# Kernel tuning notes

Hardware: AMD Instinct MI355X
Metric: run time of the kernel (lower is better)

## Reference

```python
import jax, jax.numpy as jnp
import numpy as np

N_LEAVES = 8192      # perfect binary tree, depth 13
SEQ_SIZE = 4096
EMBED = 512
NUM_CLASSES = 2


def setup_inputs() -> dict:
    key = jax.random.key(0)
    ks = jax.random.split(key, 7)
    sc = lambda n: 1.0 / np.sqrt(n)
    return {
        "leaf_seq": jax.random.normal(ks[0], (N_LEAVES, SEQ_SIZE), jnp.float32),
        # nn.Linear(sequenceSize, embedSize)
        "W_emb": jax.random.normal(ks[1], (EMBED, SEQ_SIZE), jnp.float32) * sc(SEQ_SIZE),
        "b_emb": jax.random.normal(ks[2], (EMBED,), jnp.float32) * 0.01,
        # nn.Linear(2*embedSize, embedSize)
        "W_comb": jax.random.normal(ks[3], (EMBED, 2 * EMBED), jnp.float32) * sc(2 * EMBED),
        "b_comb": jax.random.normal(ks[4], (EMBED,), jnp.float32) * 0.01,
        # nn.Linear(embedSize, numClasses)
        "W_proj": jax.random.normal(ks[5], (NUM_CLASSES, EMBED), jnp.float32) * sc(EMBED),
        "b_proj": jax.random.normal(ks[6], (NUM_CLASSES,), jnp.float32) * 0.01,
    }


def reference(leaf_seq, W_emb, b_emb, W_comb, b_comb, W_proj, b_proj):
    # Depth-batched version of the recursive traverse():
    # leaves: h = relu(embedding(seq))  -- one big GEMM instead of N batch-1 calls
    h = jax.nn.relu(leaf_seq @ W_emb.T + b_emb)            # [N_LEAVES, E]
    # internal nodes: h = relu(W(cat(left, right))), one GEMM per tree level.
    # Leaves 2i and 2i+1 are siblings (in-order perfect binary tree layout),
    # matching cat((traverse(child0), traverse(child1)), dim=1).
    while h.shape[0] > 1:                                   # fixed 13 levels at trace time
        pair = jnp.concatenate([h[0::2], h[1::2]], axis=1)  # [n/2, 2E]
        h = jax.nn.relu(pair @ W_comb.T + b_comb)           # [n/2, E]
    # root only: projection(currentNode) -> nodeProbList, cat -> [1, numClasses]
    return h @ W_proj.T + b_proj
```

## Files before the change

kernel.cpp:

```cpp
#include <hip/hip_runtime.h>
#include <stdint.h>


typedef float  f32x16 __attribute__((ext_vector_type(16)));
typedef short  s16x8  __attribute__((ext_vector_type(8)));
typedef unsigned short u16;

__device__ __forceinline__ u16 f2bf_rne(float f) {
    union { float f; uint32_t u; } v; v.f = f;
    return (u16)((v.u + 0x7FFFu + ((v.u >> 16) & 1u)) >> 16);
}
__device__ __forceinline__ float bf2f(u16 h) {
    union { uint32_t u; float f; } v; v.u = ((uint32_t)h) << 16;
    return v.f;
}
__device__ __forceinline__ void split2(float f, u16& h, u16& l) {
    union { float f; uint32_t u; } v; v.f = f;
    h = (u16)(v.u >> 16);
    union { uint32_t u; float f; } hf; hf.u = v.u & 0xFFFF0000u;
    l = f2bf_rne(f - hf.f);
}

__device__ __forceinline__ int swz(int row, int p, int e) {
    return (row * 128 + p * 64 + e) ^ ((row & 15) << 3);
}

__global__ __launch_bounds__(256) void split_kernel(
    const float* __restrict__ x, u16* __restrict__ hi, u16* __restrict__ lo, int n4)
{
    int i = blockIdx.x * 256 + threadIdx.x;
    if (i >= n4) return;
    float4 v = ((const float4*)x)[i];
    ushort4 h, l;
    split2(v.x, h.x, l.x);
    split2(v.y, h.y, l.y);
    split2(v.z, h.z, l.z);
    split2(v.w, h.w, l.w);
    ((ushort4*)hi)[i] = h;
    ((ushort4*)lo)[i] = l;
}

__global__ __launch_bounds__(256, 1) void gemm_emb(
    const float* __restrict__ Af,
    const u16* __restrict__ Bhi_g, const u16* __restrict__ Blo_g,
    const float* __restrict__ bias,
    u16* __restrict__ Chi, u16* __restrict__ Clo)
{
    constexpr int K = 4096, N = 512;
    __shared__ u16 Asw[128 * 128];
    __shared__ u16 Bsw[128 * 128];

    const int tid = threadIdx.x, wid = tid >> 6, lane = tid & 63;
    const int mb = blockIdx.x * 128, nb = blockIdx.y * 128;
    const int wm = (wid >> 1) * 64, wn = (wid & 1) * 64;
    const int sr = tid >> 1;
    const int se = (tid & 1) * 32;

    const float* pA  = Af    + (long)(mb + sr) * K + se;
    const u16*   pBh = Bhi_g + (long)(nb + sr) * K + se;
    const u16*   pBl = Blo_g + (long)(nb + sr) * K + se;

    f32x16 accA[2][2] = {};
    f32x16 accB[2][2] = {};
    float4 ra[8];
    s16x8  rbh[4], rbl[4];

    auto fetch = [&](int k0) {
#pragma unroll
        for (int i = 0; i < 8; ++i) ra[i] = *(const float4*)(pA + k0 + 4 * i);
#pragma unroll
        for (int i = 0; i < 4; ++i) {
            rbh[i] = *(const s16x8*)(pBh + k0 + 8 * i);
            rbl[i] = *(const s16x8*)(pBl + k0 + 8 * i);
        }
    };
    auto stage = [&]() {
#pragma unroll
        for (int q = 0; q < 4; ++q) {
            s16x8 hh, ll;
#pragma unroll
            for (int j = 0; j < 8; ++j) {
                float f = (j < 4) ? (&ra[2 * q].x)[j] : (&ra[2 * q + 1].x)[j - 4];
                u16 h, l; split2(f, h, l);
                hh[j] = (short)h; ll[j] = (short)l;
            }
            *(s16x8*)&Asw[swz(sr, 0, se + 8 * q)] = hh;
            *(s16x8*)&Asw[swz(sr, 1, se + 8 * q)] = ll;
            *(s16x8*)&Bsw[swz(sr, 0, se + 8 * q)] = rbh[q];
            *(s16x8*)&Bsw[swz(sr, 1, se + 8 * q)] = rbl[q];
        }
    };

    fetch(0);
    const int fr = lane & 31, ko = lane >> 5;
    for (int k0 = 0; k0 < K; k0 += 64) {
        stage();
        __syncthreads();
        if (k0 + 64 < K) fetch(k0 + 64);
#pragma unroll
        for (int s = 0; s < 4; ++s) {
            const int e = s * 16 + ko * 8;
            s16x8 ah[2], al[2], bh[2], bl[2];
#pragma unroll
            for (int i = 0; i < 2; ++i) {
                ah[i] = *(const s16x8*)&Asw[swz(wm + 32 * i + fr, 0, e)];
                al[i] = *(const s16x8*)&Asw[swz(wm + 32 * i + fr, 1, e)];
                bh[i] = *(const s16x8*)&Bsw[swz(wn + 32 * i + fr, 0, e)];
                bl[i] = *(const s16x8*)&Bsw[swz(wn + 32 * i + fr, 1, e)];
            }
#pragma unroll
            for (int i = 0; i < 2; ++i)
#pragma unroll
                for (int j = 0; j < 2; ++j) {
                    accA[i][j] = __builtin_amdgcn_mfma_f32_32x32x16_bf16(ah[i], bh[j], accA[i][j], 0, 0, 0);
                    accA[i][j] = __builtin_amdgcn_mfma_f32_32x32x16_bf16(al[i], bh[j], accA[i][j], 0, 0, 0);
                    accB[i][j] = __builtin_amdgcn_mfma_f32_32x32x16_bf16(ah[i], bl[j], accB[i][j], 0, 0, 0);
                }
        }
        __syncthreads();
    }

    const int fc = lane & 31;
#pragma unroll
    for (int i = 0; i < 2; ++i)
#pragma unroll
        for (int j = 0; j < 2; ++j) {
            const int col = nb + wn + 32 * j + fc;
            const float bv = bias[col];
#pragma unroll
            for (int reg = 0; reg < 16; ++reg) {
                const int row = mb + wm + 32 * i + (reg & 3) + 8 * (reg >> 2) + 4 * (lane >> 5);
                float v = fmaxf(accA[i][j][reg] + accB[i][j][reg] + bv, 0.f);
                u16 h = f2bf_rne(v);
                const long idx = (long)row * N + col;
                Chi[idx] = h;
                Clo[idx] = f2bf_rne(v - bf2f(h));
            }
        }
}

__global__ __launch_bounds__(256, 2) void gemm_cmb(
    const u16* __restrict__ Ahi, const u16* __restrict__ Alo,
    const u16* __restrict__ Whi, const u16* __restrict__ Wlo,
    const float* __restrict__ bias,
    u16* __restrict__ Ohi, u16* __restrict__ Olo,
    int m)
{
    constexpr int K = 1024, N = 512;
    __shared__ u16 Asw[64 * 128];
    __shared__ u16 Bsw[128 * 128];

    const int tid = threadIdx.x, wid = tid >> 6, lane = tid & 63;
    const int mb = blockIdx.x * 64, nb = blockIdx.y * 128;
    const int wm = (wid >> 1) * 32, wn = (wid & 1) * 64;
    const int ar = tid >> 2, ae = (tid & 3) * 16;
    const int br = tid >> 1, be = (tid & 1) * 32;
    const bool aval = (mb + ar) < m;
    const long aoff = (long)(mb + ar) * K + ae;
    const long boff = (long)(nb + br) * K + be;

    f32x16 accA[2] = {};
    f32x16 accB[2] = {};
    const s16x8 zz = {0, 0, 0, 0, 0, 0, 0, 0};
    s16x8 rah[2], ral[2], rbh[4], rbl[4];

    auto fetch = [&](int k0) {
        if (aval) {
            rah[0] = *(const s16x8*)(Ahi + aoff + k0);
            rah[1] = *(const s16x8*)(Ahi + aoff + k0 + 8);
            ral[0] = *(const s16x8*)(Alo + aoff + k0);
            ral[1] = *(const s16x8*)(Alo + aoff + k0 + 8);
        } else {
            rah[0] = zz; rah[1] = zz; ral[0] = zz; ral[1] = zz;
        }
#pragma unroll
        for (int i = 0; i < 4; ++i) {
            rbh[i] = *(const s16x8*)(Whi + boff + k0 + 8 * i);
            rbl[i] = *(const s16x8*)(Wlo + boff + k0 + 8 * i);
        }
    };
    auto stage = [&]() {
#pragma unroll
        for (int q = 0; q < 2; ++q) {
            *(s16x8*)&Asw[swz(ar, 0, ae + 8 * q)] = rah[q];
            *(s16x8*)&Asw[swz(ar, 1, ae + 8 * q)] = ral[q];
        }
#pragma unroll
        for (int q = 0; q < 4; ++q) {
            *(s16x8*)&Bsw[swz(br, 0, be + 8 * q)] = rbh[q];
            *(s16x8*)&Bsw[swz(br, 1, be + 8 * q)] = rbl[q];
        }
    };

    fetch(0);
    const int fr = lane & 31, ko = lane >> 5;
    for (int k0 = 0; k0 < K; k0 += 64) {
        stage();
        __syncthreads();
        if (k0 + 64 < K) fetch(k0 + 64);
#pragma unroll
        for (int s = 0; s < 4; ++s) {
            const int e = s * 16 + ko * 8;
            s16x8 ah = *(const s16x8*)&Asw[swz(wm + fr, 0, e)];
            s16x8 al = *(const s16x8*)&Asw[swz(wm + fr, 1, e)];
#pragma unroll
            for (int j = 0; j < 2; ++j) {
                s16x8 bh = *(const s16x8*)&Bsw[swz(wn + 32 * j + fr, 0, e)];
                s16x8 bl = *(const s16x8*)&Bsw[swz(wn + 32 * j + fr, 1, e)];
                accA[j] = __builtin_amdgcn_mfma_f32_32x32x16_bf16(ah, bh, accA[j], 0, 0, 0);
                accA[j] = __builtin_amdgcn_mfma_f32_32x32x16_bf16(al, bh, accA[j], 0, 0, 0);
                accB[j] = __builtin_amdgcn_mfma_f32_32x32x16_bf16(ah, bl, accB[j], 0, 0, 0);
            }
        }
        __syncthreads();
    }

    const int fc = lane & 31;
#pragma unroll
    for (int j = 0; j < 2; ++j) {
        const int col = nb + wn + 32 * j + fc;
        const float bv = bias[col];
#pragma unroll
        for (int reg = 0; reg < 16; ++reg) {
            const int row = mb + wm + (reg & 3) + 8 * (reg >> 2) + 4 * (lane >> 5);
            if (row < m) {
                float v = fmaxf(accA[j][reg] + accB[j][reg] + bv, 0.f);
                u16 h = f2bf_rne(v);
                const long idx = (long)row * N + col;
                Ohi[idx] = h;
                Olo[idx] = f2bf_rne(v - bf2f(h));
            }
        }
    }
}

__global__ __launch_bounds__(256) void tail_gemv(
    const u16* __restrict__ Hhi, const u16* __restrict__ Hlo,
    const float* __restrict__ W,
    const float* __restrict__ bias,
    u16* __restrict__ Ohi, u16* __restrict__ Olo)
{
    __shared__ float hrow[1024];
    const int row = blockIdx.x;
    const int tid = threadIdx.x;
    const int n   = blockIdx.y * 256 + tid;

    ushort4 hv = ((const ushort4*)(Hhi + (long)row * 1024))[tid];
    ushort4 lv = ((const ushort4*)(Hlo + (long)row * 1024))[tid];
    hrow[4 * tid + 0] = bf2f(hv.x) + bf2f(lv.x);
    hrow[4 * tid + 1] = bf2f(hv.y) + bf2f(lv.y);
    hrow[4 * tid + 2] = bf2f(hv.z) + bf2f(lv.z);
    hrow[4 * tid + 3] = bf2f(hv.w) + bf2f(lv.w);
    __syncthreads();

    const float* w = W + (long)n * 1024;
    float s = 0.f;
#pragma unroll 8
    for (int k = 0; k < 1024; k += 4) {
        float4 wv = *(const float4*)(w + k);
        s = fmaf(hrow[k + 0], wv.x, s);
        s = fmaf(hrow[k + 1], wv.y, s);
        s = fmaf(hrow[k + 2], wv.z, s);
        s = fmaf(hrow[k + 3], wv.w, s);
    }
    float v = fmaxf(s + bias[n], 0.f);
    u16 h = f2bf_rne(v);
    Ohi[(long)row * 512 + n] = h;
    Olo[(long)row * 512 + n] = f2bf_rne(v - bf2f(h));
}

__global__ __launch_bounds__(128) void proj_kernel(
    const u16* __restrict__ hhi, const u16* __restrict__ hlo,
    const float* __restrict__ W, const float* __restrict__ b, float* __restrict__ out)
{
    const int c    = threadIdx.x >> 6;
    const int lane = threadIdx.x & 63;
    float s = 0.f;
#pragma unroll
    for (int j = 0; j < 8; ++j) {
        const int idx = lane + 64 * j;
        s = fmaf(bf2f(hhi[idx]) + bf2f(hlo[idx]), W[c * 512 + idx], s);
    }
#pragma unroll
    for (int off = 32; off > 0; off >>= 1) s += __shfl_down(s, off);
    if (lane == 0) out[c] = s + b[c];
}

extern "C" void kernel_launch(void* const* d_in, const int* in_sizes, int n_in,
                              void* d_out, int out_size, void* d_ws, size_t ws_size,
                              hipStream_t stream)
{
    const float* leaf   = (const float*)d_in[0];
    const float* W_emb  = (const float*)d_in[1];
    const float* b_emb  = (const float*)d_in[2];
    const float* W_comb = (const float*)d_in[3];
    const float* b_comb = (const float*)d_in[4];
    const float* W_proj = (const float*)d_in[5];
    const float* b_proj = (const float*)d_in[6];
    float* out = (float*)d_out;

    u16* p = (u16*)d_ws;
    u16* WembHi  = p; p += (size_t)512 * 4096;
    u16* WembLo  = p; p += (size_t)512 * 4096;
    u16* WcombHi = p; p += (size_t)512 * 1024;
    u16* WcombLo = p; p += (size_t)512 * 1024;
    u16* h0h = p; p += (size_t)8192 * 512;
    u16* h0l = p; p += (size_t)8192 * 512;
    u16* h1h = p; p += (size_t)4096 * 512;
    u16* h1l = p; p += (size_t)4096 * 512;

    {
        int n4 = 512 * 4096 / 4;
        split_kernel<<<(n4 + 255) / 256, 256, 0, stream>>>(W_emb, WembHi, WembLo, n4);
        n4 = 512 * 1024 / 4;
        split_kernel<<<(n4 + 255) / 256, 256, 0, stream>>>(W_comb, WcombHi, WcombLo, n4);
    }

    gemm_emb<<<dim3(64, 4), 256, 0, stream>>>(
        leaf, WembHi, WembLo, b_emb, h0h, h0l);

    u16 *ih = h0h, *il = h0l, *oh = h1h, *ol = h1l;
    for (int m = 4096; m >= 64; m >>= 1) {
        gemm_cmb<<<dim3((m + 63) / 64, 4), 256, 0, stream>>>(
            ih, il, WcombHi, WcombLo, b_comb, oh, ol, m);
        u16* t;
        t = ih; ih = oh; oh = t;
        t = il; il = ol; ol = t;
    }

    for (int m = 32; m >= 1; m >>= 1) {
        tail_gemv<<<dim3(m, 2), 256, 0, stream>>>(
            ih, il, W_comb, b_comb, oh, ol);
        u16* t;
        t = ih; ih = oh; oh = t;
        t = il; il = ol; ol = t;
    }

    proj_kernel<<<1, 128, 0, stream>>>(ih, il, W_proj, b_proj, out);
}
```

Baseline: 727.4 us.

## Split-K embedding GEMM with atomics and rewrite combine GEMM as register split-K

The embedding GEMM is split into two K halves across a third grid dimension. Partial sums go into a zeroed fp32 buffer through atomic adds, and a separate reduce kernel applies bias, ReLU and the hi/lo split. The combine GEMM is rewritten to load operands straight from global memory into registers, with each wave owning a quarter of K and an LDS reduction at the end. It also uses 64x64 output tiles, so all levels down to m=1 go through the MFMA path and the tail GEMV kernels are removed. This aims to raise parallelism on the 256-block embedding GEMM and the small late levels, at the cost of atomic traffic, a memset, an extra reduce pass, workspace aliasing, and combine-kernel loads that no longer go through LDS.

```diff
diff --git a/kernel.cpp b/kernel.cpp
--- a/kernel.cpp
+++ b/kernel.cpp
@@ -43,22 +43,22 @@
 __global__ __launch_bounds__(256, 1) void gemm_emb(
     const float* __restrict__ Af,
     const u16* __restrict__ Bhi_g, const u16* __restrict__ Blo_g,
-    const float* __restrict__ bias,
-    u16* __restrict__ Chi, u16* __restrict__ Clo)
-{
-    constexpr int K = 4096, N = 512;
+    float* __restrict__ C32)
+{
+    constexpr int K = 4096, N = 512, KH = 2048;
     __shared__ u16 Asw[128 * 128];
     __shared__ u16 Bsw[128 * 128];
 
     const int tid = threadIdx.x, wid = tid >> 6, lane = tid & 63;
     const int mb = blockIdx.x * 128, nb = blockIdx.y * 128;
+    const long koff = (long)blockIdx.z * KH;
     const int wm = (wid >> 1) * 64, wn = (wid & 1) * 64;
     const int sr = tid >> 1;
     const int se = (tid & 1) * 32;
 
-    const float* pA  = Af    + (long)(mb + sr) * K + se;
-    const u16*   pBh = Bhi_g + (long)(nb + sr) * K + se;
-    const u16*   pBl = Blo_g + (long)(nb + sr) * K + se;
+    const float* pA  = Af    + (long)(mb + sr) * K + se + koff;
+    const u16*   pBh = Bhi_g + (long)(nb + sr) * K + se + koff;
+    const u16*   pBl = Blo_g + (long)(nb + sr) * K + se + koff;
 
     f32x16 accA[2][2] = {};
     f32x16 accB[2][2] = {};
@@ -93,10 +93,10 @@
 
     fetch(0);
     const int fr = lane & 31, ko = lane >> 5;
-    for (int k0 = 0; k0 < K; k0 += 64) {
+    for (int k0 = 0; k0 < KH; k0 += 64) {
         stage();
         __syncthreads();
-        if (k0 + 64 < K) fetch(k0 + 64);
+        if (k0 + 64 < KH) fetch(k0 + 64);
 #pragma unroll
         for (int s = 0; s < 4; ++s) {
             const int e = s * 16 + ko * 8;
@@ -126,147 +126,121 @@
 #pragma unroll
         for (int j = 0; j < 2; ++j) {
             const int col = nb + wn + 32 * j + fc;
-            const float bv = bias[col];
 #pragma unroll
             for (int reg = 0; reg < 16; ++reg) {
                 const int row = mb + wm + 32 * i + (reg & 3) + 8 * (reg >> 2) + 4 * (lane >> 5);
-                float v = fmaxf(accA[i][j][reg] + accB[i][j][reg] + bv, 0.f);
-                u16 h = f2bf_rne(v);
-                const long idx = (long)row * N + col;
-                Chi[idx] = h;
-                Clo[idx] = f2bf_rne(v - bf2f(h));
+                unsafeAtomicAdd(&C32[(long)row * N + col], accA[i][j][reg] + accB[i][j][reg]);
             }
         }
 }
 
-__global__ __launch_bounds__(256, 2) void gemm_cmb(
+__global__ __launch_bounds__(256) void reduce_kernel(
+    const float* __restrict__ C32, const float* __restrict__ bias,
+    u16* __restrict__ Ohi, u16* __restrict__ Olo)
+{
+    const long gid  = (long)blockIdx.x * 256 + threadIdx.x;
+    const long base = gid * 8;
+    const int  col  = (int)(base & 511);
+    float4 x0 = *(const float4*)(C32 + base);
+    float4 x1 = *(const float4*)(C32 + base + 4);
+    float4 b0 = *(const float4*)(bias + col);
+    float4 b1 = *(const float4*)(bias + col + 4);
+    float vs[8] = { x0.x + b0.x, x0.y + b0.y, x0.z + b0.z, x0.w + b0.w,
+                    x1.x + b1.x, x1.y + b1.y, x1.z + b1.z, x1.w + b1.w };
+    s16x8 oh, ol;
+#pragma unroll
+    for (int e = 0; e < 8; ++e) {
+        float v = fmaxf(vs[e], 0.f);
+        u16 h, l; split2(v, h, l);
+        oh[e] = (short)h; ol[e] = (short)l;
+    }
+    *(s16x8*)(Ohi + base) = oh;
+    *(s16x8*)(Olo + base) = ol;
+}
+
+__global__ __launch_bounds__(256) void gemm_cmb(
     const u16* __restrict__ Ahi, const u16* __restrict__ Alo,
     const u16* __restrict__ Whi, const u16* __restrict__ Wlo,
     const float* __restrict__ bias,
     u16* __restrict__ Ohi, u16* __restrict__ Olo,
     int m)
 {
-    constexpr int K = 1024, N = 512;
-    __shared__ u16 Asw[64 * 128];
-    __shared__ u16 Bsw[128 * 128];
-
+    __shared__ float red[4 * 64 * 64];
     const int tid = threadIdx.x, wid = tid >> 6, lane = tid & 63;
-    const int mb = blockIdx.x * 64, nb = blockIdx.y * 128;
-    const int wm = (wid >> 1) * 32, wn = (wid & 1) * 64;
-    const int ar = tid >> 2, ae = (tid & 3) * 16;
-    const int br = tid >> 1, be = (tid & 1) * 32;
-    const bool aval = (mb + ar) < m;
-    const long aoff = (long)(mb + ar) * K + ae;
-    const long boff = (long)(nb + br) * K + be;
-
-    f32x16 accA[2] = {};
-    f32x16 accB[2] = {};
-    const s16x8 zz = {0, 0, 0, 0, 0, 0, 0, 0};
-    s16x8 rah[2], ral[2], rbh[4], rbl[4];
-
-    auto fetch = [&](int k0) {
-        if (aval) {
-            rah[0] = *(const s16x8*)(Ahi + aoff + k0);
-            rah[1] = *(const s16x8*)(Ahi + aoff + k0 + 8);
-            ral[0] = *(const s16x8*)(Alo + aoff + k0);
-            ral[1] = *(const s16x8*)(Alo + aoff + k0 + 8);
-        } else {
-            rah[0] = zz; rah[1] = zz; ral[0] = zz; ral[1] = zz;
-        }
-#pragma unroll
-        for (int i = 0; i < 4; ++i) {
-            rbh[i] = *(const s16x8*)(Whi + boff + k0 + 8 * i);
-            rbl[i] = *(const s16x8*)(Wlo + boff + k0 + 8 * i);
-        }
-    };
-    auto stage = [&]() {
-#pragma unroll
-        for (int q = 0; q < 2; ++q) {
-            *(s16x8*)&Asw[swz(ar, 0, ae + 8 * q)] = rah[q];
-            *(s16x8*)&Asw[swz(ar, 1, ae + 8 * q)] = ral[q];
-        }
-#pragma unroll
-        for (int q = 0; q < 4; ++q) {
-            *(s16x8*)&Bsw[swz(br, 0, be + 8 * q)] = rbh[q];
-            *(s16x8*)&Bsw[swz(br, 1, be + 8 * q)] = rbl[q];
-        }
-    };
-
-    fetch(0);
-    const int fr = lane & 31, ko = lane >> 5;
-    for (int k0 = 0; k0 < K; k0 += 64) {
-        stage();
-        __syncthreads();
-        if (k0 + 64 < K) fetch(k0 + 64);
-#pragma unroll
-        for (int s = 0; s < 4; ++s) {
-            const int e = s * 16 + ko * 8;
-            s16x8 ah = *(const s16x8*)&Asw[swz(wm + fr, 0, e)];
-            s16x8 al = *(const s16x8*)&Asw[swz(wm + fr, 1, e)];
-#pragma unroll
-            for (int j = 0; j < 2; ++j) {
-                s16x8 bh = *(const s16x8*)&Bsw[swz(wn + 32 * j + fr, 0, e)];
-                s16x8 bl = *(const s16x8*)&Bsw[swz(wn + 32 * j + fr, 1, e)];
-                accA[j] = __builtin_amdgcn_mfma_f32_32x32x16_bf16(ah, bh, accA[j], 0, 0, 0);
-                accA[j] = __builtin_amdgcn_mfma_f32_32x32x16_bf16(al, bh, accA[j], 0, 0, 0);
-                accB[j] = __builtin_amdgcn_mfma_f32_32x32x16_bf16(ah, bl, accB[j], 0, 0, 0);
-            }
-        }
-        __syncthreads();
-    }
-
-    const int fc = lane & 31;
-#pragma unroll
-    for (int j = 0; j < 2; ++j) {
-        const int col = nb + wn + 32 * j + fc;
-        const float bv = bias[col];
-#pragma unroll
-        for (int reg = 0; reg < 16; ++reg) {
-            const int row = mb + wm + (reg & 3) + 8 * (reg >> 2) + 4 * (lane >> 5);
-            if (row < m) {
-                float v = fmaxf(accA[j][reg] + accB[j][reg] + bv, 0.f);
-                u16 h = f2bf_rne(v);
-                const long idx = (long)row * N + col;
-                Ohi[idx] = h;
-                Olo[idx] = f2bf_rne(v - bf2f(h));
-            }
-        }
-    }
-}
-
-__global__ __launch_bounds__(256) void tail_gemv(
-    const u16* __restrict__ Hhi, const u16* __restrict__ Hlo,
-    const float* __restrict__ W,
-    const float* __restrict__ bias,
-    u16* __restrict__ Ohi, u16* __restrict__ Olo)
-{
-    __shared__ float hrow[1024];
-    const int row = blockIdx.x;
-    const int tid = threadIdx.x;
-    const int n   = blockIdx.y * 256 + tid;
-
-    ushort4 hv = ((const ushort4*)(Hhi + (long)row * 1024))[tid];
-    ushort4 lv = ((const ushort4*)(Hlo + (long)row * 1024))[tid];
-    hrow[4 * tid + 0] = bf2f(hv.x) + bf2f(lv.x);
-    hrow[4 * tid + 1] = bf2f(hv.y) + bf2f(lv.y);
-    hrow[4 * tid + 2] = bf2f(hv.z) + bf2f(lv.z);
-    hrow[4 * tid + 3] = bf2f(hv.w) + bf2f(lv.w);
+    const int fr = lane & 31, hb = lane >> 5;
+    const int mb = blockIdx.x * 64, nb = blockIdx.y * 64;
+    const long kw = (long)wid * 256 + hb * 8;
+    const long a0 = (long)(mb + fr) * 1024 + kw;
+    const long a1 = a0 + 32 * 1024;
+    const long b0 = (long)(nb + fr) * 1024 + kw;
+    const long b1 = b0 + 32 * 1024;
+
+    f32x16 acc00 = {}, acc01 = {}, acc10 = {}, acc11 = {};
+    s16x8 Ah[2][2], Al[2][2], Bh[2][2], Bl[2][2];
+
+    Ah[0][0] = *(const s16x8*)(Ahi + a0);
+    Ah[0][1] = *(const s16x8*)(Ahi + a1);
+    Al[0][0] = *(const s16x8*)(Alo + a0);
+    Al[0][1] = *(const s16x8*)(Alo + a1);
+    Bh[0][0] = *(const s16x8*)(Whi + b0);
+    Bh[0][1] = *(const s16x8*)(Whi + b1);
+    Bl[0][0] = *(const s16x8*)(Wlo + b0);
+    Bl[0][1] = *(const s16x8*)(Wlo + b1);
+
+#pragma unroll
+    for (int s = 0; s < 16; ++s) {
+        const int cur = s & 1, nxt = cur ^ 1;
+        if (s + 1 < 16) {
+            const int ko = (s + 1) * 16;
+            Ah[nxt][0] = *(const s16x8*)(Ahi + a0 + ko);
+            Ah[nxt][1] = *(const s16x8*)(Ahi + a1 + ko);
+            Al[nxt][0] = *(const s16x8*)(Alo + a0 + ko);
+            Al[nxt][1] = *(const s16x8*)(Alo + a1 + ko);
+            Bh[nxt][0] = *(const s16x8*)(Whi + b0 + ko);
+            Bh[nxt][1] = *(const s16x8*)(Whi + b1 + ko);
+            Bl[nxt][0] = *(const s16x8*)(Wlo + b0 + ko);
+            Bl[nxt][1] = *(const s16x8*)(Wlo + b1 + ko);
+        }
+        acc00 = __builtin_amdgcn_mfma_f32_32x32x16_bf16(Ah[cur][0], Bh[cur][0], acc00, 0, 0, 0);
+        acc01 = __builtin_amdgcn_mfma_f32_32x32x16_bf16(Ah[cur][0], Bh[cur][1], acc01, 0, 0, 0);
+        acc10 = __builtin_amdgcn_mfma_f32_32x32x16_bf16(Ah[cur][1], Bh[cur][0], acc10, 0, 0, 0);
+        acc11 = __builtin_amdgcn_mfma_f32_32x32x16_bf16(Ah[cur][1], Bh[cur][1], acc11, 0, 0, 0);
+        acc00 = __builtin_amdgcn_mfma_f32_32x32x16_bf16(Al[cur][0], Bh[cur][0], acc00, 0, 0, 0);
+        acc01 = __builtin_amdgcn_mfma_f32_32x32x16_bf16(Al[cur][0], Bh[cur][1], acc01, 0, 0, 0);
+        acc10 = __builtin_amdgcn_mfma_f32_32x32x16_bf16(Al[cur][1], Bh[cur][0], acc10, 0, 0, 0);
+        acc11 = __builtin_amdgcn_mfma_f32_32x32x16_bf16(Al[cur][1], Bh[cur][1], acc11, 0, 0, 0);
+        acc00 = __builtin_amdgcn_mfma_f32_32x32x16_bf16(Ah[cur][0], Bl[cur][0], acc00, 0, 0, 0);
+        acc01 = __builtin_amdgcn_mfma_f32_32x32x16_bf16(Ah[cur][0], Bl[cur][1], acc01, 0, 0, 0);
+        acc10 = __builtin_amdgcn_mfma_f32_32x32x16_bf16(Ah[cur][1], Bl[cur][0], acc10, 0, 0, 0);
+        acc11 = __builtin_amdgcn_mfma_f32_32x32x16_bf16(Ah[cur][1], Bl[cur][1], acc11, 0, 0, 0);
+    }
+
+    float* my = red + wid * 4096;
+#pragma unroll
+    for (int reg = 0; reg < 16; ++reg) {
+        const int rr = (reg & 3) + 8 * (reg >> 2) + 4 * hb;
+        my[rr * 64 + fr]             = acc00[reg];
+        my[rr * 64 + 32 + fr]        = acc01[reg];
+        my[(32 + rr) * 64 + fr]      = acc10[reg];
+        my[(32 + rr) * 64 + 32 + fr] = acc11[reg];
+    }
     __syncthreads();
 
-    const float* w = W + (long)n * 1024;
-    float s = 0.f;
-#pragma unroll 8
-    for (int k = 0; k < 1024; k += 4) {
-        float4 wv = *(const float4*)(w + k);
-        s = fmaf(hrow[k + 0], wv.x, s);
-        s = fmaf(hrow[k + 1], wv.y, s);
-        s = fmaf(hrow[k + 2], wv.z, s);
-        s = fmaf(hrow[k + 3], wv.w, s);
-    }
-    float v = fmaxf(s + bias[n], 0.f);
-    u16 h = f2bf_rne(v);
-    Ohi[(long)row * 512 + n] = h;
-    Olo[(long)row * 512 + n] = f2bf_rne(v - bf2f(h));
+    const int c = tid & 63, rq = (tid >> 6) * 16;
+    const float bv = bias[nb + c];
+#pragma unroll
+    for (int k = 0; k < 16; ++k) {
+        const int r = rq + k;
+        const int grow = mb + r;
+        if (grow < m) {
+            const int o = r * 64 + c;
+            float sum = red[o] + red[4096 + o] + red[8192 + o] + red[12288 + o];
+            float v = fmaxf(sum + bv, 0.f);
+            u16 h, l; split2(v, h, l);
+            Ohi[(long)grow * 512 + nb + c] = h;
+            Olo[(long)grow * 512 + nb + c] = l;
+        }
+    }
 }
 
 __global__ __launch_bounds__(128) void proj_kernel(
@@ -300,41 +274,36 @@
     float* out = (float*)d_out;
 
     u16* p = (u16*)d_ws;
-    u16* WembHi  = p; p += (size_t)512 * 4096;
-    u16* WembLo  = p; p += (size_t)512 * 4096;
-    u16* WcombHi = p; p += (size_t)512 * 1024;
-    u16* WcombLo = p; p += (size_t)512 * 1024;
-    u16* h0h = p; p += (size_t)8192 * 512;
-    u16* h0l = p; p += (size_t)8192 * 512;
-    u16* h1h = p; p += (size_t)4096 * 512;
-    u16* h1l = p; p += (size_t)4096 * 512;
-
-    {
-        int n4 = 512 * 4096 / 4;
-        split_kernel<<<(n4 + 255) / 256, 256, 0, stream>>>(W_emb, WembHi, WembLo, n4);
-        n4 = 512 * 1024 / 4;
-        split_kernel<<<(n4 + 255) / 256, 256, 0, stream>>>(W_comb, WcombHi, WcombLo, n4);
-    }
-
-    gemm_emb<<<dim3(64, 4), 256, 0, stream>>>(
-        leaf, WembHi, WembLo, b_emb, h0h, h0l);
+    u16* r0 = p;
+    u16* r1 = p + 8388608;
+    u16* r2 = p + 9437184;
+
+    u16* WembHi  = r0;
+    u16* WembLo  = r0 + 2097152;
+    u16* h0h     = r0;
+    u16* h0l     = r0 + 4194304;
+    u16* WcombHi = r1;
+    u16* WcombLo = r1 + 524288;
+    float* C32   = (float*)r2;
+    u16* h1h     = r2;
+    u16* h1l     = r2 + 2097152;
+
+    hipMemsetAsync((void*)C32, 0, (size_t)4194304 * 4, stream);
+
+    split_kernel<<<2048, 256, 0, stream>>>(W_emb, WembHi, WembLo, 524288);
+    split_kernel<<<512, 256, 0, stream>>>(W_comb, WcombHi, WcombLo, 131072);
+
+    gemm_emb<<<dim3(64, 4, 2), 256, 0, stream>>>(leaf, WembHi, WembLo, C32);
+    reduce_kernel<<<2048, 256, 0, stream>>>(C32, b_emb, h0h, h0l);
 
     u16 *ih = h0h, *il = h0l, *oh = h1h, *ol = h1l;
-    for (int m = 4096; m >= 64; m >>= 1) {
-        gemm_cmb<<<dim3((m + 63) / 64, 4), 256, 0, stream>>>(
+    for (int m = 4096; m >= 1; m >>= 1) {
+        gemm_cmb<<<dim3((m + 63) / 64, 8), 256, 0, stream>>>(
             ih, il, WcombHi, WcombLo, b_comb, oh, ol, m);
         u16* t;
         t = ih; ih = oh; oh = t;
         t = il; il = ol; ol = t;
     }
 
-    for (int m = 32; m >= 1; m >>= 1) {
-        tail_gemv<<<dim3(m, 2), 256, 0, stream>>>(
-            ih, il, W_comb, b_comb, oh, ol);
-        u16* t;
-        t = ih; ih = oh; oh = t;
-        t = il; il = ol; ol = t;
-    }
-
     proj_kernel<<<1, 128, 0, stream>>>(ih, il, W_proj, b_proj, out);
 }
```

Result: faster. 639.2 us (-12.1%).
